# Kernel optimization log

Measured on AMD Instinct MI355X. Metric: run time of the kernel, lower is better.

## Reference

```python
import jax, jax.numpy as jnp
import numpy as np

NUM_HEADS = 16
D_MODEL = 1024
D_K = D_MODEL // NUM_HEADS


def setup_inputs() -> dict:
    key = jax.random.key(0)
    ks = jax.random.split(key, 6)
    B, S = 4, 2048
    x = jax.random.normal(ks[0], (B, S, D_MODEL), dtype=jnp.float32)
    scale = 1.0 / np.sqrt(D_MODEL)
    W_q = jax.random.normal(ks[1], (D_MODEL, D_MODEL), dtype=jnp.float32) * scale
    W_k = jax.random.normal(ks[2], (D_MODEL, D_MODEL), dtype=jnp.float32) * scale
    W_v = jax.random.normal(ks[3], (D_MODEL, D_MODEL), dtype=jnp.float32) * scale
    W_o = jax.random.normal(ks[4], (D_MODEL, D_MODEL), dtype=jnp.float32) * scale
    b_o = jnp.zeros((D_MODEL,), dtype=jnp.float32)
    return {"x": x, "W_q": W_q, "W_k": W_k, "W_v": W_v, "W_o": W_o, "b_o": b_o}


def reference(x, W_q, W_k, W_v, W_o, b_o):
    B, S, D = x.shape
    H, dk = NUM_HEADS, D_K
    # torch nn.Linear computes x @ W.T
    q = (x @ W_q.T).reshape(B, S, H, dk).transpose(0, 2, 1, 3)  # [B,H,S,dk]
    k = (x @ W_k.T).reshape(B, S, H, dk).transpose(0, 2, 1, 3)
    v = (x @ W_v.T).reshape(B, S, H, dk).transpose(0, 2, 1, 3)
    scores = jnp.einsum('bhqd,bhkd->bhqk', q, k) / jnp.sqrt(jnp.float32(dk))
    causal = jnp.tril(jnp.ones((S, S), dtype=bool))  # allowed positions
    scores = jnp.where(causal[None, None], scores, -jnp.inf)
    attn = jax.nn.softmax(scores, axis=-1)
    out = jnp.einsum('bhqk,bhkd->bhqd', attn, v)
    combined = out.transpose(0, 2, 1, 3).reshape(B, S, D)
    return combined @ W_o.T + b_o
```

## Files before the change

### kernel.cpp

```cpp
#include <hip/hip_runtime.h>

typedef __attribute__((ext_vector_type(8))) short short8;
typedef __attribute__((ext_vector_type(4))) float f32x4;

#define GLOAD16(gp, lp)                                                        \
  __builtin_amdgcn_global_load_lds(                                            \
      (const __attribute__((address_space(1))) void*)(gp),                     \
      (__attribute__((address_space(3))) void*)(lp), 16, 0, 0)

__device__ __forceinline__ unsigned short f2bf(float f) {
  unsigned int u = __builtin_bit_cast(unsigned int, f);
  u += 0x7fffu + ((u >> 16) & 1u);
  return (unsigned short)(u >> 16);
}

__global__ __launch_bounds__(256) void cvt_f32_bf16(
    const float* __restrict__ src, unsigned short* __restrict__ dst, int n,
    float scale) {
  int i = (blockIdx.x * 256 + threadIdx.x) * 8;
  if (i + 8 <= n) {
    float4 a = *(const float4*)(src + i);
    float4 b = *(const float4*)(src + i + 4);
    short8 r;
    r[0] = (short)f2bf(a.x * scale); r[1] = (short)f2bf(a.y * scale);
    r[2] = (short)f2bf(a.z * scale); r[3] = (short)f2bf(a.w * scale);
    r[4] = (short)f2bf(b.x * scale); r[5] = (short)f2bf(b.y * scale);
    r[6] = (short)f2bf(b.z * scale); r[7] = (short)f2bf(b.w * scale);
    *(short8*)(dst + i) = r;
  }
}

__global__ __launch_bounds__(256) void cvt_w4(
    const float* __restrict__ Wq, const float* __restrict__ Wk,
    const float* __restrict__ Wv, const float* __restrict__ Wo,
    unsigned short* __restrict__ Wqkv, unsigned short* __restrict__ Wob,
    int DD, float qscale) {
  const int y = blockIdx.y;
  const float* src = (y == 0) ? Wq : (y == 1) ? Wk : (y == 2) ? Wv : Wo;
  unsigned short* dst = (y < 3) ? Wqkv + (size_t)y * DD : Wob;
  const float scale = (y == 0) ? qscale : 1.0f;
  int i = (blockIdx.x * 256 + threadIdx.x) * 8;
  if (i + 8 <= DD) {
    float4 a = *(const float4*)(src + i);
    float4 b = *(const float4*)(src + i + 4);
    short8 r;
    r[0] = (short)f2bf(a.x * scale); r[1] = (short)f2bf(a.y * scale);
    r[2] = (short)f2bf(a.z * scale); r[3] = (short)f2bf(a.w * scale);
    r[4] = (short)f2bf(b.x * scale); r[5] = (short)f2bf(b.y * scale);
    r[6] = (short)f2bf(b.z * scale); r[7] = (short)f2bf(b.w * scale);
    *(short8*)(dst + i) = r;
  }
}

template <int BN, int OUTF32>
__global__ __launch_bounds__(512) void gemm_nt2(
    const unsigned short* __restrict__ A, const unsigned short* __restrict__ B,
    void* __restrict__ Cout, const float* __restrict__ bias, int M, int N,
    int K, int nwg_y) {
  constexpr int NF = BN / 64;
  constexpr int WNSZ = BN / 4;
  __shared__ __align__(16) unsigned short As[2][256][64];
  __shared__ __align__(16) unsigned short Bs[2][BN][64];

  const int nwg = gridDim.x;
  const int id = blockIdx.x;
  const int sw = (id & 7) * (nwg >> 3) + (id >> 3);
  const int bx = sw / nwg_y, by = sw % nwg_y;
  const int row0 = bx * 256, col0 = by * BN;

  const int tid = threadIdx.x;
  const int wave = tid >> 6, lane = tid & 63;
  const int wm = wave >> 2, wn = wave & 3;
  const int l15 = lane & 15, l16 = lane >> 4;
  const int lrow = lane >> 3, lcol = (lane & 7) * 8;
  const int wv8 = wave * 8;

  f32x4 acc[8][NF];
#pragma unroll
  for (int m = 0; m < 8; ++m)
#pragma unroll
    for (int n = 0; n < NF; ++n) acc[m][n] = f32x4{0.f, 0.f, 0.f, 0.f};

  const int nt = K >> 6;

#define STAGE_TILE(buf, k0)                                                    \
  {                                                                            \
    _Pragma("unroll") for (int j = 0; j < 4; ++j) {                            \
      const unsigned short* gp =                                               \
          A + (size_t)(row0 + j * 64 + wv8 + lrow) * K + (k0) + lcol;          \
      GLOAD16(gp, &As[buf][j * 64 + wv8][0]);                                  \
    }                                                                          \
    _Pragma("unroll") for (int j = 0; j < NF; ++j) {                           \
      const unsigned short* gp =                                               \
          B + (size_t)(col0 + j * 64 + wv8 + lrow) * K + (k0) + lcol;          \
      GLOAD16(gp, &Bs[buf][j * 64 + wv8][0]);                                  \
    }                                                                          \
  }

  STAGE_TILE(0, 0)
  __syncthreads();

  for (int t = 0; t < nt; ++t) {
    const int cur = t & 1;
    if (t + 1 < nt) STAGE_TILE(cur ^ 1, (t + 1) << 6)

#pragma unroll
    for (int kk = 0; kk < 2; ++kk) {
      short8 a[8], b[NF];
#pragma unroll
      for (int m = 0; m < 8; ++m)
        a[m] = *(const short8*)&As[cur][wm * 128 + m * 16 + l15][kk * 32 + l16 * 8];
#pragma unroll
      for (int n = 0; n < NF; ++n)
        b[n] = *(const short8*)&Bs[cur][wn * WNSZ + n * 16 + l15][kk * 32 + l16 * 8];
#pragma unroll
      for (int m = 0; m < 8; ++m)
#pragma unroll
        for (int n = 0; n < NF; ++n)
          acc[m][n] =
              __builtin_amdgcn_mfma_f32_16x16x32_bf16(a[m], b[n], acc[m][n], 0, 0, 0);
    }
    __syncthreads();
  }

#pragma unroll
  for (int m = 0; m < 8; ++m) {
    const int row = row0 + wm * 128 + m * 16 + l16 * 4;
#pragma unroll
    for (int n = 0; n < NF; ++n) {
      const int col = col0 + wn * WNSZ + n * 16 + l15;
      float bv = 0.f;
      if (OUTF32) bv = bias[col];
#pragma unroll
      for (int r = 0; r < 4; ++r) {
        const float v = acc[m][n][r] + bv;
        if (OUTF32)
          ((float*)Cout)[(size_t)(row + r) * N + col] = v;
        else
          ((unsigned short*)Cout)[(size_t)(row + r) * N + col] = f2bf(v);
      }
    }
  }
#undef STAGE_TILE
}

__global__ __launch_bounds__(512) void attn_fwd(
    const unsigned short* __restrict__ QKV, unsigned short* __restrict__ AO) {
  const int S = 2048, LD = 3072;
  const int qt = gridDim.x - 1 - blockIdx.x;
  const int bh = blockIdx.y, b = bh >> 4, h = bh & 15;
  const int tid = threadIdx.x, wave = tid >> 6, lane = tid & 63;
  const int l15 = lane & 15, l16 = lane >> 4;
  const int q0 = qt * 128;

  __shared__ __align__(16) char KsB[2][64 * 128];
  __shared__ __align__(16) char VTB[2][64 * 128];
  __shared__ __align__(16) char PlB[8][16 * 128];

  const unsigned short* qptr =
      QKV + (size_t)(b * S + q0 + wave * 16 + l15) * LD + h * 64 + l16 * 8;
  short8 qf[2];
  qf[0] = *(const short8*)(qptr);
  qf[1] = *(const short8*)(qptr + 32);

  const int krow = lane >> 3;
  const int kcol = (((lane & 7) ^ (lane >> 3)) & 7) * 8;
  const int vp_ = tid & 31, vd0 = ((tid >> 5) & 7) * 8;

  float mrow = -1e30f, lsum = 0.f;
  f32x4 accO[4] = {};
  const int nkv = 2 * qt + 2;

  {
    if (wave >= 4) {
#pragma unroll
      for (int i = 0; i < 2; ++i) {
        const int c = (wave - 4) * 2 + i;
        const unsigned short* gp =
            QKV + (size_t)(b * S + c * 8 + krow) * LD + 1024 + h * 64 + kcol;
        GLOAD16(gp, KsB[0] + c * 1024);
      }
    } else {
      const unsigned short* vp =
          QKV + (size_t)(b * S + 2 * vp_) * LD + 2048 + h * 64 + vd0;
      short8 va = *(const short8*)vp;
      short8 vb = *(const short8*)(vp + LD);
      uint4 vaw = __builtin_bit_cast(uint4, va);
      uint4 vbw = __builtin_bit_cast(uint4, vb);
      const unsigned int aw[4] = {vaw.x, vaw.y, vaw.z, vaw.w};
      const unsigned int bw[4] = {vbw.x, vbw.y, vbw.z, vbw.w};
#pragma unroll
      for (int w = 0; w < 4; ++w) {
        unsigned int e = __builtin_amdgcn_perm(bw[w], aw[w], 0x05040100u);
        unsigned int o = __builtin_amdgcn_perm(bw[w], aw[w], 0x07060302u);
        *(unsigned int*)(VTB[0] + (((vd0 + 2 * w) * 128 + 4 * vp_) ^ ((2 * w) << 4))) = e;
        *(unsigned int*)(VTB[0] + (((vd0 + 2 * w + 1) * 128 + 4 * vp_) ^ ((2 * w + 1) << 4))) = o;
      }
    }
  }
  __syncthreads();

  for (int t = 0; t < nkv; ++t) {
    const int cur = t & 1, kv0 = t * 64;

    f32x4 accS[4] = {};
#pragma unroll
    for (int sub = 0; sub < 4; ++sub) {
      const int rw = sub * 16 + l15;
#pragma unroll
      for (int kk = 0; kk < 2; ++kk) {
        short8 kf = *(const short8*)(KsB[cur] + rw * 128 +
                                     ((kk * 64 + l16 * 16) ^ ((l15 & 7) << 4)));
        accS[sub] =
            __builtin_amdgcn_mfma_f32_16x16x32_bf16(kf, qf[kk], accS[sub], 0, 0, 0);
      }
    }

    short8 va, vb;
    const bool pre = (t + 1 < nkv);
    if (pre) {
      const int kvn = kv0 + 64;
      if (wave >= 4) {
#pragma unroll
        for (int i = 0; i < 2; ++i) {
          const int c = (wave - 4) * 2 + i;
          const unsigned short* gp =
              QKV + (size_t)(b * S + kvn + c * 8 + krow) * LD + 1024 + h * 64 + kcol;
          GLOAD16(gp, KsB[cur ^ 1] + c * 1024);
        }
      } else {
        const unsigned short* vp =
            QKV + (size_t)(b * S + kvn + 2 * vp_) * LD + 2048 + h * 64 + vd0;
        va = *(const short8*)vp;
        vb = *(const short8*)(vp + LD);
      }
    }

    const bool nm = (kv0 + 63 > q0 + wave * 16);
    float mx = -1e30f;
    if (nm) {
      const int qabs = q0 + wave * 16 + l15;
#pragma unroll
      for (int sub = 0; sub < 4; ++sub)
#pragma unroll
        for (int r = 0; r < 4; ++r) {
          float s = accS[sub][r];
          if (kv0 + sub * 16 + l16 * 4 + r > qabs) s = -1e30f;
          accS[sub][r] = s;
          mx = fmaxf(mx, s);
        }
    } else {
#pragma unroll
      for (int sub = 0; sub < 4; ++sub)
#pragma unroll
        for (int r = 0; r < 4; ++r) mx = fmaxf(mx, accS[sub][r]);
    }
    mx = fmaxf(mx, __shfl_xor(mx, 16));
    mx = fmaxf(mx, __shfl_xor(mx, 32));

    if (__any(mx > mrow + 8.0f)) {
      const float mnew = fmaxf(mrow, mx);
      const float alpha = exp2f(mrow - mnew);
      mrow = mnew;
      lsum *= alpha;
      float al[4];
#pragma unroll
      for (int r = 0; r < 4; ++r) al[r] = __shfl(alpha, l16 * 4 + r);
#pragma unroll
      for (int sd = 0; sd < 4; ++sd)
#pragma unroll
        for (int r = 0; r < 4; ++r) accO[sd][r] *= al[r];
    }

    float rs = 0.f;
#pragma unroll
    for (int sub = 0; sub < 4; ++sub) {
      float p0 = exp2f(accS[sub][0] - mrow);
      float p1 = exp2f(accS[sub][1] - mrow);
      float p2 = exp2f(accS[sub][2] - mrow);
      float p3 = exp2f(accS[sub][3] - mrow);
      rs += (p0 + p1) + (p2 + p3);
      unsigned int pk01, pk23;
      asm("v_cvt_pk_bf16_f32 %0, %1, %2" : "=v"(pk01) : "v"(p0), "v"(p1));
      asm("v_cvt_pk_bf16_f32 %0, %1, %2" : "=v"(pk23) : "v"(p2), "v"(p3));
      uint2 pw = {pk01, pk23};
      *(uint2*)(PlB[wave] +
                ((l15 * 128 + sub * 32 + l16 * 8) ^ ((l15 & 7) << 4))) = pw;
    }
    rs += __shfl_xor(rs, 16);
    rs += __shfl_xor(rs, 32);
    lsum += rs;

    if (pre && wave < 4) {
      uint4 vaw = __builtin_bit_cast(uint4, va);
      uint4 vbw = __builtin_bit_cast(uint4, vb);
      const unsigned int aw[4] = {vaw.x, vaw.y, vaw.z, vaw.w};
      const unsigned int bw[4] = {vbw.x, vbw.y, vbw.z, vbw.w};
#pragma unroll
      for (int w = 0; w < 4; ++w) {
        unsigned int e = __builtin_amdgcn_perm(bw[w], aw[w], 0x05040100u);
        unsigned int o = __builtin_amdgcn_perm(bw[w], aw[w], 0x07060302u);
        *(unsigned int*)(VTB[cur ^ 1] +
                         (((vd0 + 2 * w) * 128 + 4 * vp_) ^ ((2 * w) << 4))) = e;
        *(unsigned int*)(VTB[cur ^ 1] +
                         (((vd0 + 2 * w + 1) * 128 + 4 * vp_) ^ ((2 * w + 1) << 4))) = o;
      }
    }

#pragma unroll
    for (int kk = 0; kk < 2; ++kk) {
      short8 pf = *(const short8*)(PlB[wave] + ((l15 * 128 + kk * 64 + l16 * 16) ^
                                               ((l15 & 7) << 4)));
#pragma unroll
      for (int sd = 0; sd < 4; ++sd) {
        short8 vf = *(const short8*)(VTB[cur] + (sd * 16 + l15) * 128 +
                                     ((kk * 64 + l16 * 16) ^ ((l15 & 7) << 4)));
        accO[sd] =
            __builtin_amdgcn_mfma_f32_16x16x32_bf16(pf, vf, accO[sd], 0, 0, 0);
      }
    }
    __syncthreads();
  }

  float ls[4];
#pragma unroll
  for (int r = 0; r < 4; ++r) ls[r] = __shfl(lsum, l16 * 4 + r);
#pragma unroll
  for (int sd = 0; sd < 4; ++sd)
#pragma unroll
    for (int r = 0; r < 4; ++r) {
      AO[(size_t)(b * S + q0 + wave * 16 + l16 * 4 + r) * 1024 + h * 64 +
         sd * 16 + l15] = f2bf(accO[sd][r] / ls[r]);
    }
}

extern "C" void kernel_launch(void* const* d_in, const int* in_sizes, int n_in,
                              void* d_out, int out_size, void* d_ws,
                              size_t ws_size, hipStream_t stream) {
  const float* x = (const float*)d_in[0];
  const float* Wq = (const float*)d_in[1];
  const float* Wk = (const float*)d_in[2];
  const float* Wv = (const float*)d_in[3];
  const float* Wo = (const float*)d_in[4];
  const float* bo = (const float*)d_in[5];

  char* ws = (char*)d_ws;
  unsigned short* xb = (unsigned short*)(ws);
  unsigned short* Wqkv = (unsigned short*)(ws + (size_t)(16 << 20));
  unsigned short* Wob = (unsigned short*)(ws + (size_t)(22 << 20));
  unsigned short* QKV = (unsigned short*)(ws + (size_t)(24 << 20));
  unsigned short* AO = (unsigned short*)(ws + (size_t)(72 << 20));

  const int M = 8192, D = 1024;
  const float QSCALE = 0.125f * 1.44269504088896340736f;

  cvt_f32_bf16<<<M * D / 2048, 256, 0, stream>>>(x, xb, M * D, 1.0f);
  dim3 gw(D * D / 2048, 4);
  cvt_w4<<<gw, 256, 0, stream>>>(Wq, Wk, Wv, Wo, Wqkv, Wob, D * D, QSCALE);

  gemm_nt2<192, 0><<<(M / 256) * (3072 / 192), 512, 0, stream>>>(
      xb, Wqkv, QKV, nullptr, M, 3072, D, 3072 / 192);

  dim3 g2(16, 64);
  attn_fwd<<<g2, 512, 0, stream>>>(QKV, AO);

  gemm_nt2<128, 1><<<(M / 256) * (D / 128), 512, 0, stream>>>(
      AO, Wob, d_out, bo, M, D, D, D / 128);
}
```

Measured before the change: 329.2 us.

## Keep attention probabilities in registers by permuting K rows and transposing PV MFMA

Loads K rows into shared memory in a permuted order, so each lane's S-accumulator entries line up with the B-operand layout of the PV MFMA. The probabilities then pack straight into register fragments and the per-wave shared-memory staging buffer and its reads go away. The PV MFMA operands are swapped so the output is transposed, which removes the alpha and lsum shuffles. The final store now writes packed bf16 pairs, normalised by a reciprocal. The causal mask indices are remapped to match the permuted K order, and any error in that mapping would silently give wrong results.

```diff
diff --git a/kernel.cpp b/kernel.cpp
--- a/kernel.cpp
+++ b/kernel.cpp
@@ -144,6 +144,11 @@
 #undef STAGE_TILE
 }
 
+__device__ __forceinline__ int kvperm(int slot) {
+  const int s = slot >> 4, l = (slot >> 2) & 3, rr = slot & 3;
+  return 32 * (s & 1) + 8 * l + 4 * (s >> 1) + rr;
+}
+
 __global__ __launch_bounds__(512) void attn_fwd(
     const unsigned short* __restrict__ QKV, unsigned short* __restrict__ AO) {
   const int S = 2048, LD = 3072;
@@ -155,7 +160,6 @@
 
   __shared__ __align__(16) char KsB[2][64 * 128];
   __shared__ __align__(16) char VTB[2][64 * 128];
-  __shared__ __align__(16) char PlB[8][16 * 128];
 
   const unsigned short* qptr =
       QKV + (size_t)(b * S + q0 + wave * 16 + l15) * LD + h * 64 + l16 * 8;
@@ -165,11 +169,16 @@
 
   const int krow = lane >> 3;
   const int kcol = (((lane & 7) ^ (lane >> 3)) & 7) * 8;
+  int kvp[2];
+#pragma unroll
+  for (int i = 0; i < 2; ++i)
+    kvp[i] = kvperm(((wave - 4) * 2 + i) * 8 + krow);
   const int vp_ = tid & 31, vd0 = ((tid >> 5) & 7) * 8;
 
   float mrow = -1e30f, lsum = 0.f;
   f32x4 accO[4] = {};
   const int nkv = 2 * qt + 2;
+  const int koff8 = 8 * l16;
 
   {
     if (wave >= 4) {
@@ -177,7 +186,7 @@
       for (int i = 0; i < 2; ++i) {
         const int c = (wave - 4) * 2 + i;
         const unsigned short* gp =
-            QKV + (size_t)(b * S + c * 8 + krow) * LD + 1024 + h * 64 + kcol;
+            QKV + (size_t)(b * S + kvp[i]) * LD + 1024 + h * 64 + kcol;
         GLOAD16(gp, KsB[0] + c * 1024);
       }
     } else {
@@ -225,7 +234,7 @@
         for (int i = 0; i < 2; ++i) {
           const int c = (wave - 4) * 2 + i;
           const unsigned short* gp =
-              QKV + (size_t)(b * S + kvn + c * 8 + krow) * LD + 1024 + h * 64 + kcol;
+              QKV + (size_t)(b * S + kvn + kvp[i]) * LD + 1024 + h * 64 + kcol;
           GLOAD16(gp, KsB[cur ^ 1] + c * 1024);
         }
       } else {
@@ -241,14 +250,16 @@
     if (nm) {
       const int qabs = q0 + wave * 16 + l15;
 #pragma unroll
-      for (int sub = 0; sub < 4; ++sub)
+      for (int sub = 0; sub < 4; ++sub) {
+        const int kbase = kv0 + 32 * (sub & 1) + 4 * (sub >> 1) + koff8;
 #pragma unroll
         for (int r = 0; r < 4; ++r) {
           float s = accS[sub][r];
-          if (kv0 + sub * 16 + l16 * 4 + r > qabs) s = -1e30f;
+          if (kbase + r > qabs) s = -1e30f;
           accS[sub][r] = s;
           mx = fmaxf(mx, s);
         }
+      }
     } else {
 #pragma unroll
       for (int sub = 0; sub < 4; ++sub)
@@ -263,33 +274,36 @@
       const float alpha = exp2f(mrow - mnew);
       mrow = mnew;
       lsum *= alpha;
-      float al[4];
-#pragma unroll
-      for (int r = 0; r < 4; ++r) al[r] = __shfl(alpha, l16 * 4 + r);
 #pragma unroll
       for (int sd = 0; sd < 4; ++sd)
 #pragma unroll
-        for (int r = 0; r < 4; ++r) accO[sd][r] *= al[r];
+        for (int r = 0; r < 4; ++r) accO[sd][r] *= alpha;
     }
 
     float rs = 0.f;
 #pragma unroll
-    for (int sub = 0; sub < 4; ++sub) {
-      float p0 = exp2f(accS[sub][0] - mrow);
-      float p1 = exp2f(accS[sub][1] - mrow);
-      float p2 = exp2f(accS[sub][2] - mrow);
-      float p3 = exp2f(accS[sub][3] - mrow);
-      rs += (p0 + p1) + (p2 + p3);
-      unsigned int pk01, pk23;
-      asm("v_cvt_pk_bf16_f32 %0, %1, %2" : "=v"(pk01) : "v"(p0), "v"(p1));
-      asm("v_cvt_pk_bf16_f32 %0, %1, %2" : "=v"(pk23) : "v"(p2), "v"(p3));
-      uint2 pw = {pk01, pk23};
-      *(uint2*)(PlB[wave] +
-                ((l15 * 128 + sub * 32 + l16 * 8) ^ ((l15 & 7) << 4))) = pw;
-    }
+    for (int sub = 0; sub < 4; ++sub)
+#pragma unroll
+      for (int r = 0; r < 4; ++r) {
+        const float pv = exp2f(accS[sub][r] - mrow);
+        accS[sub][r] = pv;
+        rs += pv;
+      }
     rs += __shfl_xor(rs, 16);
     rs += __shfl_xor(rs, 32);
     lsum += rs;
+
+    short8 pf[2];
+#pragma unroll
+    for (int kk = 0; kk < 2; ++kk) {
+      unsigned int w0, w1, w2, w3;
+      asm("v_cvt_pk_bf16_f32 %0, %1, %2" : "=v"(w0) : "v"(accS[kk][0]), "v"(accS[kk][1]));
+      asm("v_cvt_pk_bf16_f32 %0, %1, %2" : "=v"(w1) : "v"(accS[kk][2]), "v"(accS[kk][3]));
+      asm("v_cvt_pk_bf16_f32 %0, %1, %2" : "=v"(w2) : "v"(accS[kk + 2][0]), "v"(accS[kk + 2][1]));
+      asm("v_cvt_pk_bf16_f32 %0, %1, %2" : "=v"(w3) : "v"(accS[kk + 2][2]), "v"(accS[kk + 2][3]));
+      uint4 u = {w0, w1, w2, w3};
+      pf[kk] = __builtin_bit_cast(short8, u);
+    }
 
     if (pre && wave < 4) {
       uint4 vaw = __builtin_bit_cast(uint4, va);
@@ -309,29 +323,31 @@
 
 #pragma unroll
     for (int kk = 0; kk < 2; ++kk) {
-      short8 pf = *(const short8*)(PlB[wave] + ((l15 * 128 + kk * 64 + l16 * 16) ^
-                                               ((l15 & 7) << 4)));
 #pragma unroll
       for (int sd = 0; sd < 4; ++sd) {
         short8 vf = *(const short8*)(VTB[cur] + (sd * 16 + l15) * 128 +
                                      ((kk * 64 + l16 * 16) ^ ((l15 & 7) << 4)));
         accO[sd] =
-            __builtin_amdgcn_mfma_f32_16x16x32_bf16(pf, vf, accO[sd], 0, 0, 0);
+            __builtin_amdgcn_mfma_f32_16x16x32_bf16(vf, pf[kk], accO[sd], 0, 0, 0);
       }
     }
     __syncthreads();
   }
 
-  float ls[4];
-#pragma unroll
-  for (int r = 0; r < 4; ++r) ls[r] = __shfl(lsum, l16 * 4 + r);
-#pragma unroll
-  for (int sd = 0; sd < 4; ++sd)
-#pragma unroll
-    for (int r = 0; r < 4; ++r) {
-      AO[(size_t)(b * S + q0 + wave * 16 + l16 * 4 + r) * 1024 + h * 64 +
-         sd * 16 + l15] = f2bf(accO[sd][r] / ls[r]);
-    }
+  const float inv = __builtin_amdgcn_rcpf(lsum);
+  unsigned short* aop =
+      AO + (size_t)(b * S + q0 + wave * 16 + l15) * 1024 + h * 64;
+#pragma unroll
+  for (int sd = 0; sd < 4; ++sd) {
+    const int d = sd * 16 + l16 * 4;
+    unsigned int w0, w1;
+    float o0 = accO[sd][0] * inv, o1 = accO[sd][1] * inv;
+    float o2 = accO[sd][2] * inv, o3 = accO[sd][3] * inv;
+    asm("v_cvt_pk_bf16_f32 %0, %1, %2" : "=v"(w0) : "v"(o0), "v"(o1));
+    asm("v_cvt_pk_bf16_f32 %0, %1, %2" : "=v"(w1) : "v"(o2), "v"(o3));
+    *(unsigned int*)(aop + d) = w0;
+    *(unsigned int*)(aop + d + 2) = w1;
+  }
 }
 
 extern "C" void kernel_launch(void* const* d_in, const int* in_sizes, int n_in,
```

Measured after the change: 322.3 us. 1.02x faster.
